# Kernel optimization log

Hardware: AMD Instinct MI355X
Metric: run time of the kernel (lower is better)

## Reference

```python
import jax, jax.numpy as jnp
import numpy as np
from jax import lax

RADIUS = [1, 3, 5, 9, 13, 21]
RATE = 1
K = 4            # shift radius -> (2K+1)^2 = 81 shifts
EPS = 1e-8       # torch.cosine_similarity eps


def setup_inputs() -> dict:
    key = jax.random.key(0)
    k1, k2, k3, k4 = jax.random.split(key, 4)
    b, cin, cout, h, w = 2, 128, 128, 96, 128
    x = jax.random.normal(k1, (b, cout, h, w), dtype=jnp.float32)
    y = jax.random.normal(k2, (b, cin, h, w), dtype=jnp.float32)
    # 6 dilated conv branches, all Conv2d(cin, cout, 3) -> stacked (6, O, I, 3, 3)
    weights = jax.random.normal(k3, (6, cout, cin, 3, 3), dtype=jnp.float32) * 0.05
    biases = jax.random.normal(k4, (6, cout), dtype=jnp.float32) * 0.05
    return {"x": x, "y": y, "weights": weights, "biases": biases}


def _forward(x, y, weights, biases):
    b, c, h, w = y.shape
    k = K
    # reflect-pad y by k, then 'same' dilated convs (zero padding = dilation)
    y_pad = jnp.pad(y, ((0, 0), (0, 0), (k, k), (k, k)), mode="reflect")

    # precompute grouped query features and their norms once
    xg = x.reshape(b, 4, -1, h, w)                      # (b,4,c/4,h,w)
    xn = jnp.sqrt(jnp.sum(xg * xg, axis=2))             # (b,4,h,w)

    # per-branch conv outputs over the padded extent, grouped, with cached norms
    branches = []
    for idx, r in enumerate(RADIUS):
        d = r * RATE
        yo = lax.conv_general_dilated(
            y_pad, weights[idx], window_strides=(1, 1),
            padding=[(d, d), (d, d)], rhs_dilation=(d, d),
            dimension_numbers=("NCHW", "OIHW", "NCHW"),
        ) + biases[idx][None, :, None, None]            # (b,cout,h+2k,w+2k)
        yg = yo.reshape(b, 4, -1, h + 2 * k, w + 2 * k)
        yn = jnp.sqrt(jnp.sum(yg * yg, axis=2))          # (b,4,h+2k,w+2k)
        branches.append((yg, yn))

    result = []
    for i in range(-k, k + 1):
        for j in range(-k, k + 1):
            sx, sy = k + i, k + j
            corrs = []
            for yg, yn in branches:
                ygs = yg[:, :, :, sx:sx + h, sy:sy + w]
                yns = yn[:, :, sx:sx + h, sy:sy + w]
                dot = jnp.einsum("bgchw,bgchw->bghw", xg, ygs)
                corrs.append(dot / jnp.maximum(xn * yns, EPS))
            result.append(jnp.concatenate(corrs, axis=1))  # (b,24,h,w)
    return jnp.stack(result, axis=2)                       # (b,24,81,h,w)


def reference(x, y, weights, biases):
    return _forward(x, y, weights, biases)
```

## Files before the change

kernel.cpp:

```cpp
#include <hip/hip_runtime.h>
#include <math.h>

#define B 2
#define CH 128
#define H 96
#define W 128
#define HP 104
#define WP 136
#define KPAD 4
#define NSHIFT 81
#define NBR 6
#define HW (H*W)
#define HWP (HP*WP)
#define NTILE 111

typedef _Float16 h2 __attribute__((ext_vector_type(2)));
typedef _Float16 half8 __attribute__((ext_vector_type(8)));
typedef float floatx4 __attribute__((ext_vector_type(4)));

__device__ __constant__ int d_radius[NBR] = {1, 3, 5, 9, 13, 21};

__device__ __forceinline__ void async16(const _Float16* g, _Float16* l) {
    __builtin_amdgcn_global_load_lds(
        (const __attribute__((address_space(1))) unsigned int*)g,
        (__attribute__((address_space(3))) unsigned int*)l, 16, 0, 0);
}

__global__ __launch_bounds__(256) void prep_y(const float* __restrict__ y,
                                              _Float16* __restrict__ yt16) {
    __shared__ h2 tile[64 * 129];
    const int tid = threadIdx.x;
    const int b = blockIdx.y;
    const int pix0 = blockIdx.x * 128;
    const int half = tid >> 7;
    const int pl = tid & 127;

    const float* yb = y + (size_t)b * CH * HW + pix0 + pl;
    #pragma unroll
    for (int k = 0; k < 32; ++k) {
        int c = half * 64 + 2 * k;
        float v0 = yb[(size_t)c * HW];
        float v1 = yb[(size_t)(c + 1) * HW];
        h2 v; v[0] = (_Float16)v0; v[1] = (_Float16)v1;
        tile[(half * 32 + k) * 129 + pl] = v;
    }
    __syncthreads();

    _Float16* ob = yt16 + ((size_t)b * HW + pix0) * CH;
    #pragma unroll
    for (int it = 0; it < 8; ++it) {
        int pix = it * 16 + (tid >> 4);
        int c2b = (tid & 15) * 4;
        h2 t0 = tile[(c2b + 0) * 129 + pix];
        h2 t1 = tile[(c2b + 1) * 129 + pix];
        h2 t2 = tile[(c2b + 2) * 129 + pix];
        h2 t3 = tile[(c2b + 3) * 129 + pix];
        half8 o;
        o[0] = t0[0]; o[1] = t0[1]; o[2] = t1[0]; o[3] = t1[1];
        o[4] = t2[0]; o[5] = t2[1]; o[6] = t3[0]; o[7] = t3[1];
        *(half8*)(ob + (size_t)pix * CH + (tid & 15) * 8) = o;
    }
}

__global__ __launch_bounds__(256) void convert_w_kernel(const float* __restrict__ w,
                                                        _Float16* __restrict__ w16t,
                                                        _Float16* __restrict__ zbuf) {
    int gid = blockIdx.x * 256 + threadIdx.x;
    if (gid < 256) zbuf[gid] = (_Float16)0.0f;
    if (gid >= NBR * 9 * CH * CH) return;
    int ci = gid & 127;
    int co = (gid >> 7) & 127;
    int rest = gid >> 14;
    int tap = rest % 9;
    int br = rest / 9;
    w16t[gid] = (_Float16)w[(((size_t)(br * CH + co)) * CH + ci) * 9 + tap];
}

__global__ __launch_bounds__(256) void prep_x(const float* __restrict__ x,
                                              h2* __restrict__ xh,
                                              float* __restrict__ xn) {
    const int b = blockIdx.y;
    const int pix = blockIdx.x * 256 + threadIdx.x;
    const float* xb = x + (size_t)b * CH * HW + pix;
    #pragma unroll
    for (int g = 0; g < 4; ++g) {
        float s = 0.f;
        #pragma unroll
        for (int p = 0; p < 16; ++p) {
            int c = g * 32 + 2 * p;
            float v0 = xb[(size_t)c * HW];
            float v1 = xb[(size_t)(c + 1) * HW];
            h2 v; v[0] = (_Float16)v0; v[1] = (_Float16)v1;
            xh[((size_t)((b * 4 + g) * 16 + p)) * HW + pix] = v;
            s += v0 * v0 + v1 * v1;
        }
        xn[(size_t)(b * 4 + g) * HW + pix] = sqrtf(s);
    }
}

__global__ __launch_bounds__(256) void conv_mfma(const _Float16* __restrict__ yt16,
                                                 const _Float16* __restrict__ w16t,
                                                 const _Float16* __restrict__ zbuf,
                                                 const float* __restrict__ biases,
                                                 h2* __restrict__ ygh,
                                                 float* __restrict__ yn_all) {
    const int tid = threadIdx.x;
    const int lane = tid & 63;
    const int wv = tid >> 6;
    const int tile = blockIdx.x;
    const int br = blockIdx.y;
    const int b = blockIdx.z;
    const int d = d_radius[br];
    const int px0 = tile * 128;

    __shared__ __align__(16) _Float16 Al[2][128 * 32];
    __shared__ __align__(16) _Float16 Bl[2][128 * 32];

    const int l16 = tid & 3;
    int ph[2], pw[2];
    bool pval[2];
    #pragma unroll
    for (int s = 0; s < 2; ++s) {
        int pixl = s * 64 + (tid >> 2);
        int pix = px0 + pixl;
        pval[s] = pix < HWP;
        int phh = pix / WP;
        ph[s] = phh; pw[s] = pix - phh * WP;
    }

    const _Float16* ytb = yt16 + (size_t)b * HW * CH;
    const _Float16* wbr = w16t + (size_t)br * 9 * CH * CH;

    floatx4 acc[4][4];
    #pragma unroll
    for (int i = 0; i < 4; i++)
        #pragma unroll
        for (int j = 0; j < 4; j++) {
            floatx4 z = {0.f, 0.f, 0.f, 0.f};
            acc[i][j] = z;
        }

    const int mrow = (wv & 1) * 64 + (lane & 15);
    const int ncol = (wv >> 1) * 64 + (lane & 15);
    const int kq = (lane >> 4) * 8;

    auto comp_brow = [&](int tap, const _Float16*& o0, const _Float16*& o1) {
        const int dkh = (tap / 3 - 1) * d;
        const int dkw = (tap % 3 - 1) * d;
        const _Float16* bw[2];
        #pragma unroll
        for (int s = 0; s < 2; ++s) {
            int gr = ph[s] + dkh, gc = pw[s] + dkw;
            bool v = pval[s] && ((unsigned)gr < (unsigned)HP) && ((unsigned)gc < (unsigned)WP);
            if (v) {
                int yr = gr - KPAD; yr = yr < 0 ? -yr : (yr >= H ? 2 * (H - 1) - yr : yr);
                int yc = gc - KPAD; yc = yc < 0 ? -yc : (yc >= W ? 2 * (W - 1) - yc : yc);
                bw[s] = ytb + ((size_t)(yr * W + yc)) * CH + l16 * 8;
            } else {
                bw[s] = zbuf + l16 * 8;
            }
        }
        o0 = bw[0]; o1 = bw[1];
    };

    const _Float16* bc0; const _Float16* bc1;
    comp_brow(0, bc0, bc1);
    const _Float16* wa = wbr + (tid >> 2) * CH + l16 * 8;

    async16(wa,           Al[0] + wv * 512);
    async16(wa + 64 * CH, Al[0] + 2048 + wv * 512);
    async16(bc0,          Bl[0] + wv * 512);
    async16(bc1,          Bl[0] + 2048 + wv * 512);
    __syncthreads();

    for (int tap = 0; tap < 9; ++tap) {
        const _Float16* bn0 = bc0; const _Float16* bn1 = bc1;
        #pragma unroll
        for (int ck = 0; ck < 4; ++ck) {
            const int cur = ck & 1;
            const int nxt = cur ^ 1;
            if (ck < 3) {
                const int ci0 = (ck + 1) * 32;
                async16(wa + ci0,           Al[nxt] + wv * 512);
                async16(wa + 64 * CH + ci0, Al[nxt] + 2048 + wv * 512);
                async16(bc0 + ci0,          Bl[nxt] + wv * 512);
                async16(bc1 + ci0,          Bl[nxt] + 2048 + wv * 512);
            } else if (tap < 8) {
                comp_brow(tap + 1, bn0, bn1);
                async16(wa + CH * CH,           Al[nxt] + wv * 512);
                async16(wa + CH * CH + 64 * CH, Al[nxt] + 2048 + wv * 512);
                async16(bn0,                    Bl[nxt] + wv * 512);
                async16(bn1,                    Bl[nxt] + 2048 + wv * 512);
            }
            half8 af[4], bf[4];
            #pragma unroll
            for (int i = 0; i < 4; i++) af[i] = *(const half8*)&Al[cur][(mrow + i * 16) * 32 + kq];
            #pragma unroll
            for (int j = 0; j < 4; j++) bf[j] = *(const half8*)&Bl[cur][(ncol + j * 16) * 32 + kq];
            #pragma unroll
            for (int i = 0; i < 4; i++)
                #pragma unroll
                for (int j = 0; j < 4; j++)
                    acc[i][j] = __builtin_amdgcn_mfma_f32_16x16x32_f16(af[i], bf[j], acc[i][j], 0, 0, 0);
            __syncthreads();
        }
        bc0 = bn0; bc1 = bn1;
        wa += CH * CH;
    }

    float yna[2][4];
    #pragma unroll
    for (int gs = 0; gs < 2; ++gs)
        #pragma unroll
        for (int j = 0; j < 4; ++j) yna[gs][j] = 0.f;

    #pragma unroll
    for (int i = 0; i < 4; i++) {
        int m0 = (wv & 1) * 64 + i * 16 + (lane >> 4) * 4;
        int g0 = (m0 >> 5);
        int pp = (m0 & 31) >> 1;
        float b0 = biases[br * CH + m0];
        float b1 = biases[br * CH + m0 + 1];
        float b2 = biases[br * CH + m0 + 2];
        float b3 = biases[br * CH + m0 + 3];
        h2* outp = ygh + (((size_t)(br * B + b) * 4 + g0) * 16 + pp) * HWP;
        #pragma unroll
        for (int j = 0; j < 4; j++) {
            int pix = px0 + (wv >> 1) * 64 + j * 16 + (lane & 15);
            if (pix < HWP) {
                float f0 = acc[i][j][0] + b0;
                float f1 = acc[i][j][1] + b1;
                float f2 = acc[i][j][2] + b2;
                float f3 = acc[i][j][3] + b3;
                yna[i >> 1][j] += f0 * f0 + f1 * f1 + f2 * f2 + f3 * f3;
                h2 v0, v1;
                v0[0] = (_Float16)f0;
                v0[1] = (_Float16)f1;
                v1[0] = (_Float16)f2;
                v1[1] = (_Float16)f3;
                outp[pix] = v0;
                outp[(size_t)HWP + pix] = v1;
            }
        }
    }

    #pragma unroll
    for (int gs = 0; gs < 2; ++gs) {
        #pragma unroll
        for (int j = 0; j < 4; ++j) {
            float s = yna[gs][j];
            s += __shfl_xor(s, 16);
            s += __shfl_xor(s, 32);
            if ((lane >> 4) == 0) {
                int pix = px0 + (wv >> 1) * 64 + j * 16 + lane;
                if (pix < HWP) {
                    int g = (wv & 1) * 2 + gs;
                    yn_all[((size_t)((br * B + b) * 4 + g)) * HWP + pix] = sqrtf(s);
                }
            }
        }
    }
}

#define CPAIR 4
__global__ __launch_bounds__(256) void corr2_kernel(const h2* __restrict__ xh,
                                                    const h2* __restrict__ ygh,
                                                    const float* __restrict__ xn,
                                                    const float* __restrict__ yn_all,
                                                    float* __restrict__ out) {
    const int tid = threadIdx.x;
    const int row = tid >> 5;
    const int col4 = (tid & 31) * 4;
    const int H0 = blockIdx.x * 8;
    const int bg = blockIdx.y;
    const int g = bg & 3, b = bg >> 2;
    const int brl = blockIdx.z / 3;
    const int chunk = blockIdx.z - brl * 3;
    const int hh = H0 + row;
    const int row0 = H0 + chunk * 3;

    __shared__ __align__(16) _Float16 yt[2][CPAIR * 340 * 8];

    const h2* ygb = ygh + ((size_t)((brl * B + b) * 4 + g) * 16) * HWP;
    const h2* xb  = xh  + ((size_t)(b * 4 + g) * 16) * HW;
    const float* ynb = yn_all + (size_t)((brl * B + b) * 4 + g) * HWP;

    float xnv[4];
    *(floatx4*)xnv = *(const floatx4*)(xn + (size_t)(b * 4 + g) * HW + hh * W + col4);

    float acc[108];
    #pragma unroll
    for (int s = 0; s < 108; ++s) acc[s] = 0.f;

    for (int i = tid; i < CPAIR * 340; i += 256) {
        int pr = i / 340, off = i - pr * 340;
        const _Float16* src =
            (const _Float16*)(ygb + (size_t)pr * HWP + row0 * WP) + off * 8;
        async16(src, yt[0] + i * 8);
    }
    __syncthreads();

    #pragma unroll
    for (int pi = 0; pi < 4; ++pi) {
        const int cur = pi & 1;
        if (pi < 3) {
            const int p0n = (pi + 1) * CPAIR;
            for (int i = tid; i < CPAIR * 340; i += 256) {
                int pr = i / 340, off = i - pr * 340;
                const _Float16* src =
                    (const _Float16*)(ygb + (size_t)(p0n + pr) * HWP + row0 * WP) + off * 8;
                async16(src, yt[cur ^ 1] + i * 8);
            }
        }
        const int p0 = pi * CPAIR;
        #pragma unroll
        for (int cp = 0; cp < CPAIR; ++cp) {
            h2 x2[4];
            *(half8*)x2 = *(const half8*)(xb + (size_t)(p0 + cp) * HW + hh * W + col4);
            #pragma unroll
            for (int sx = 0; sx < 3; ++sx) {
                h2 yv[12];
                const _Float16* yr = yt[cur] + (cp * 1360 + (row + sx) * 136 + col4) * 2;
                ((half8*)yv)[0] = *(const half8*)(yr);
                ((half8*)yv)[1] = *(const half8*)(yr + 8);
                ((half8*)yv)[2] = *(const half8*)(yr + 16);
                #pragma unroll
                for (int sy = 0; sy < 9; ++sy)
                    #pragma unroll
                    for (int j = 0; j < 4; ++j)
                        acc[(sx * 9 + sy) * 4 + j] = __builtin_amdgcn_fdot2(
                            x2[j], yv[sy + j], acc[(sx * 9 + sy) * 4 + j], false);
            }
        }
        __syncthreads();
    }

    #pragma unroll
    for (int sxl = 0; sxl < 3; ++sxl) {
        int sx = chunk * 3 + sxl;
        float ynv[12];
        const float* yp = ynb + (size_t)(hh + sx) * WP + col4;
        *(floatx4*)&ynv[0] = *(const floatx4*)(yp);
        *(floatx4*)&ynv[4] = *(const floatx4*)(yp + 4);
        *(floatx4*)&ynv[8] = *(const floatx4*)(yp + 8);
        float* ob = out + ((size_t)(b * 24 + brl * 4 + g) * NSHIFT + sx * 9) * HW
                    + hh * W + col4;
        #pragma unroll
        for (int sy = 0; sy < 9; ++sy) {
            float o[4];
            #pragma unroll
            for (int j = 0; j < 4; ++j) {
                float den = xnv[j] * ynv[j + sy];
                den = den > 1e-8f ? den : 1e-8f;
                o[j] = acc[(sxl * 9 + sy) * 4 + j] / den;
            }
            *(floatx4*)(ob + (size_t)sy * HW) = *(floatx4*)o;
        }
    }
}

extern "C" void kernel_launch(void* const* d_in, const int* in_sizes, int n_in,
                              void* d_out, int out_size, void* d_ws, size_t ws_size,
                              hipStream_t stream) {
    const float* x       = (const float*)d_in[0];
    const float* y       = (const float*)d_in[1];
    const float* weights = (const float*)d_in[2];
    const float* biases  = (const float*)d_in[3];
    float* out = (float*)d_out;

    const size_t ygh_b = (size_t)NBR * B * 4 * 16 * HWP * 4;
    const size_t yn_b  = (size_t)NBR * B * 4 * HWP * 4;
    const size_t xn_b  = (size_t)B * 4 * HW * 4;
    const size_t yt_b  = (size_t)B * HW * CH * 2;
    const size_t wt_b  = (size_t)NBR * 9 * CH * CH * 2;
    const size_t xh_b  = (size_t)B * 4 * 16 * HW * 4;

    char* p = (char*)d_ws;
    h2* ygh       = (h2*)p;       p += ygh_b;
    float* yn_all = (float*)p;    p += yn_b;
    float* xn     = (float*)p;    p += xn_b;
    _Float16* yt16 = (_Float16*)p; p += yt_b;
    _Float16* w16t = (_Float16*)p; p += wt_b;
    h2* xh        = (h2*)p;       p += xh_b;
    _Float16* zbuf = (_Float16*)p;

    prep_y<<<dim3(HW / 128, B), 256, 0, stream>>>(y, yt16);
    convert_w_kernel<<<(NBR * 9 * CH * CH + 255) / 256, 256, 0, stream>>>(weights, w16t, zbuf);
    prep_x<<<dim3(HW / 256, B), 256, 0, stream>>>(x, xh, xn);

    conv_mfma<<<dim3(NTILE, NBR, B), 256, 0, stream>>>(yt16, w16t, zbuf, biases, ygh, yn_all);

    corr2_kernel<<<dim3(12, 8, NBR * 3), 256, 0, stream>>>(xh, ygh, xn, yn_all, out);
}
```

Measured before the change: 354.8 us.

## Triple-buffer conv MFMA loads and remap blocks with XCD-aware swizzle

The conv kernel now flattens its grid and maps each block index through a stride-8 swizzle. Work items that share a tile (all branches and batches) therefore land on the same XCD, which should improve L2 reuse of the y input. The K loop moves from double buffering with a full barrier per step to a 3-stage LDS ring. Loads for step s+2 are issued before computing step s, with explicit vmcnt waits and raw s_barrier. This keeps two loads in flight and lowers stall time, at the cost of 50% more LDS, which may reduce occupancy.

Result: no change. 356.4 us (+0.5%).

```diff
diff --git a/kernel.cpp b/kernel.cpp
--- a/kernel.cpp
+++ b/kernel.cpp
@@ -13,6 +13,8 @@
 #define HW (H*W)
 #define HWP (HP*WP)
 #define NTILE 111
+#define NWORK (NTILE*12)
+#define NBLK  (8*167)
 
 typedef _Float16 h2 __attribute__((ext_vector_type(2)));
 typedef _Float16 half8 __attribute__((ext_vector_type(8)));
@@ -104,17 +106,22 @@
                                                  const float* __restrict__ biases,
                                                  h2* __restrict__ ygh,
                                                  float* __restrict__ yn_all) {
+    const int f = blockIdx.x;
+    const int Wk = (f & 7) * 167 + (f >> 3);
+    if (Wk >= NWORK) return;
+    const int tile = Wk / 12;
+    const int brb = Wk - tile * 12;
+    const int br = brb >> 1;
+    const int b = brb & 1;
+
     const int tid = threadIdx.x;
     const int lane = tid & 63;
     const int wv = tid >> 6;
-    const int tile = blockIdx.x;
-    const int br = blockIdx.y;
-    const int b = blockIdx.z;
     const int d = d_radius[br];
     const int px0 = tile * 128;
 
-    __shared__ __align__(16) _Float16 Al[2][128 * 32];
-    __shared__ __align__(16) _Float16 Bl[2][128 * 32];
+    __shared__ __align__(16) _Float16 Al[3][128 * 32];
+    __shared__ __align__(16) _Float16 Bl[3][128 * 32];
 
     const int l16 = tid & 3;
     int ph[2], pw[2];
@@ -144,7 +151,8 @@
     const int ncol = (wv >> 1) * 64 + (lane & 15);
     const int kq = (lane >> 4) * 8;
 
-    auto comp_brow = [&](int tap, const _Float16*& o0, const _Float16*& o1) {
+    const _Float16* bt0; const _Float16* bt1;
+    auto comp_brow = [&](int tap) {
         const int dkh = (tap / 3 - 1) * d;
         const int dkw = (tap % 3 - 1) * d;
         const _Float16* bw[2];
@@ -160,53 +168,55 @@
                 bw[s] = zbuf + l16 * 8;
             }
         }
-        o0 = bw[0]; o1 = bw[1];
+        bt0 = bw[0]; bt1 = bw[1];
     };
 
-    const _Float16* bc0; const _Float16* bc1;
-    comp_brow(0, bc0, bc1);
-    const _Float16* wa = wbr + (tid >> 2) * CH + l16 * 8;
-
-    async16(wa,           Al[0] + wv * 512);
-    async16(wa + 64 * CH, Al[0] + 2048 + wv * 512);
-    async16(bc0,          Bl[0] + wv * 512);
-    async16(bc1,          Bl[0] + 2048 + wv * 512);
-    __syncthreads();
-
-    for (int tap = 0; tap < 9; ++tap) {
-        const _Float16* bn0 = bc0; const _Float16* bn1 = bc1;
-        #pragma unroll
-        for (int ck = 0; ck < 4; ++ck) {
-            const int cur = ck & 1;
-            const int nxt = cur ^ 1;
-            if (ck < 3) {
-                const int ci0 = (ck + 1) * 32;
-                async16(wa + ci0,           Al[nxt] + wv * 512);
-                async16(wa + 64 * CH + ci0, Al[nxt] + 2048 + wv * 512);
-                async16(bc0 + ci0,          Bl[nxt] + wv * 512);
-                async16(bc1 + ci0,          Bl[nxt] + 2048 + wv * 512);
-            } else if (tap < 8) {
-                comp_brow(tap + 1, bn0, bn1);
-                async16(wa + CH * CH,           Al[nxt] + wv * 512);
-                async16(wa + CH * CH + 64 * CH, Al[nxt] + 2048 + wv * 512);
-                async16(bn0,                    Bl[nxt] + wv * 512);
-                async16(bn1,                    Bl[nxt] + 2048 + wv * 512);
-            }
-            half8 af[4], bf[4];
+    const _Float16* wa0 = wbr + (tid >> 2) * CH + l16 * 8;
+    auto issue = [&](int t, int bufi) {
+        const int tap = t >> 2, ck = t & 3;
+        const int ci0 = ck * 32;
+        const _Float16* wa = wa0 + tap * (CH * CH) + ci0;
+        async16(wa,           Al[bufi] + wv * 512);
+        async16(wa + 64 * CH, Al[bufi] + 2048 + wv * 512);
+        async16(bt0 + ci0,    Bl[bufi] + wv * 512);
+        async16(bt1 + ci0,    Bl[bufi] + 2048 + wv * 512);
+    };
+
+    auto compute = [&](int bufi) {
+        half8 af[4], bf[4];
+        #pragma unroll
+        for (int i = 0; i < 4; i++) af[i] = *(const half8*)&Al[bufi][(mrow + i * 16) * 32 + kq];
+        #pragma unroll
+        for (int j = 0; j < 4; j++) bf[j] = *(const half8*)&Bl[bufi][(ncol + j * 16) * 32 + kq];
+        #pragma unroll
+        for (int i = 0; i < 4; i++)
             #pragma unroll
-            for (int i = 0; i < 4; i++) af[i] = *(const half8*)&Al[cur][(mrow + i * 16) * 32 + kq];
-            #pragma unroll
-            for (int j = 0; j < 4; j++) bf[j] = *(const half8*)&Bl[cur][(ncol + j * 16) * 32 + kq];
-            #pragma unroll
-            for (int i = 0; i < 4; i++)
-                #pragma unroll
-                for (int j = 0; j < 4; j++)
-                    acc[i][j] = __builtin_amdgcn_mfma_f32_16x16x32_f16(af[i], bf[j], acc[i][j], 0, 0, 0);
-            __syncthreads();
-        }
-        bc0 = bn0; bc1 = bn1;
-        wa += CH * CH;
-    }
+            for (int j = 0; j < 4; j++)
+                acc[i][j] = __builtin_amdgcn_mfma_f32_16x16x32_f16(af[i], bf[j], acc[i][j], 0, 0, 0);
+    };
+
+    comp_brow(0);
+    issue(0, 0);
+    issue(1, 1);
+
+    int bufc = 0;
+    for (int s = 0; s < 35; ++s) {
+        asm volatile("s_waitcnt vmcnt(4)" ::: "memory");
+        __builtin_amdgcn_s_barrier();
+        __builtin_amdgcn_sched_barrier(0);
+        const int t2 = s + 2;
+        if (t2 < 36) {
+            if ((t2 & 3) == 0) comp_brow(t2 >> 2);
+            int bn = bufc + 2; if (bn >= 3) bn -= 3;
+            issue(t2, bn);
+        }
+        compute(bufc);
+        bufc = (bufc == 2) ? 0 : bufc + 1;
+    }
+    asm volatile("s_waitcnt vmcnt(0)" ::: "memory");
+    __builtin_amdgcn_s_barrier();
+    __builtin_amdgcn_sched_barrier(0);
+    compute(bufc);
 
     float yna[2][4];
     #pragma unroll
@@ -388,7 +398,7 @@
     convert_w_kernel<<<(NBR * 9 * CH * CH + 255) / 256, 256, 0, stream>>>(weights, w16t, zbuf);
     prep_x<<<dim3(HW / 256, B), 256, 0, stream>>>(x, xh, xn);
 
-    conv_mfma<<<dim3(NTILE, NBR, B), 256, 0, stream>>>(yt16, w16t, zbuf, biases, ygh, yn_all);
+    conv_mfma<<<dim3(NBLK), 256, 0, stream>>>(yt16, w16t, zbuf, biases, ygh, yn_all);
 
     corr2_kernel<<<dim3(12, 8, NBR * 3), 256, 0, stream>>>(xh, ygh, xn, yn_all, out);
 }
```
